# Performance work log

Hardware: AMD Instinct MI355X
Metric: run time of the kernel (lower is better)

Reference implementation:

```python
import jax, jax.numpy as jnp
import numpy as np

GAMMA = 2
EPS = 1e-8  # torch F.cosine_similarity norm clamp


def setup_inputs() -> dict:
    key = jax.random.key(0)
    k1, k2, k3 = jax.random.split(key, 3)
    b, c, h, w = 32, 256, 32, 32
    x = jax.random.normal(k1, (b, c, h, w), dtype=jnp.float32)
    # 1x1 conv transform_net (num_layers=1): weight (c_out, c_in), bias (c_out,)
    conv_w = jax.random.normal(k2, (c, c), dtype=jnp.float32) / np.sqrt(c)
    conv_b = jax.random.normal(k3, (c,), dtype=jnp.float32) * 0.01
    return {"x": x, "conv_w": conv_w, "conv_b": conv_b}


def reference(x, conv_w, conv_b):
    b, c, h, w = x.shape
    hw = h * w
    xf = x.reshape(b, c, hw)  # (b, c, hw)
    # cosine similarity: normalize channels once, then a single GEMM
    norm = jnp.sqrt(jnp.sum(xf * xf, axis=1, keepdims=True))
    xn = xf / jnp.maximum(norm, EPS)
    sim = jnp.einsum('bcq,bck->bqk', xn, xn)  # (b, hw, hw)
    sim = jax.nn.relu(sim) ** GAMMA
    # 1x1 conv transform
    t = jnp.einsum('oc,bck->bok', conv_w, xf) + conv_b[None, :, None]  # (b, c, hw)
    # weighted aggregation: out[b, c, q] = sum_k sim[b, q, k] * t[b, c, k]
    out = jnp.einsum('bqk,bck->bcq', sim, t)
    return out.reshape(b, c, h, w)
```

## Files before the change

### kernel.cpp

```cpp
#include <hip/hip_runtime.h>
#include <math.h>

#define B 32
#define C 256
#define HW 1024

typedef __attribute__((ext_vector_type(8))) short bf16x8;
typedef __attribute__((ext_vector_type(4))) float f32x4;

__device__ __forceinline__ unsigned short f2bf(float f) {
    unsigned int u = __float_as_uint(f);
    u += 0x7fffu + ((u >> 16) & 1u);
    return (unsigned short)(u >> 16);
}

__device__ __forceinline__ void gload16(const void* g, void* l) {
    __builtin_amdgcn_global_load_lds(
        (const __attribute__((address_space(1))) unsigned int*)g,
        (__attribute__((address_space(3))) unsigned int*)l, 16, 0, 0);
}

__global__ __launch_bounds__(256) void prepn_kernel(const float* __restrict__ x,
                                                    float* __restrict__ norm,
                                                    unsigned short* __restrict__ xnT) {
    __shared__ float xt[256][65];
    __shared__ float psum[4][64];
    __shared__ float rn[64];
    const int t = threadIdx.x;
    const int q0 = blockIdx.x * 64, b = blockIdx.y;
    const float* xb = x + (size_t)b * C * HW + q0;
#pragma unroll
    for (int p = 0; p < 16; ++p) {
        int u = p * 256 + t;
        int c = u >> 4, q4 = (u & 15) * 4;
        float4 v = *(const float4*)(xb + (size_t)c * HW + q4);
        xt[c][q4] = v.x; xt[c][q4 + 1] = v.y; xt[c][q4 + 2] = v.z; xt[c][q4 + 3] = v.w;
    }
    __syncthreads();
    {
        int cb = t >> 6, q = t & 63;
        float s = 0.f;
#pragma unroll
        for (int cc = 0; cc < 64; ++cc) {
            float v = xt[cb * 64 + cc][q];
            s += v * v;
        }
        psum[cb][q] = s;
    }
    __syncthreads();
    if (t < 64) {
        float s = psum[0][t] + psum[1][t] + psum[2][t] + psum[3][t];
        float n = fmaxf(sqrtf(s), 1e-8f);
        norm[b * HW + q0 + t] = n;
        rn[t] = 1.f / n;
    }
    __syncthreads();
    unsigned short* xrow = xnT + ((size_t)b * HW + q0) * C;
#pragma unroll
    for (int p = 0; p < 16; ++p) {
        int q = p * 4 + (t >> 6);
        float rnq = rn[q];
#pragma unroll
        for (int i = 0; i < 4; ++i) {
            int c = (t & 63) + 64 * i;
            xrow[(size_t)q * C + c] = f2bf(xt[c][q] * rnq);
        }
    }
}

__global__ __launch_bounds__(256) void castw_kernel(const float* __restrict__ w,
                                                    unsigned short* __restrict__ wb) {
    int i = (blockIdx.x * 256 + threadIdx.x) * 4;
    float4 v = *(const float4*)(w + i);
    unsigned long long pk = (unsigned long long)f2bf(v.x) |
                            ((unsigned long long)f2bf(v.y) << 16) |
                            ((unsigned long long)f2bf(v.z) << 32) |
                            ((unsigned long long)f2bf(v.w) << 48);
    *(unsigned long long*)(wb + i) = pk;
}

__global__ __launch_bounds__(256) void tgemm_kernel(
    const unsigned short* __restrict__ A, const unsigned short* __restrict__ Bm,
    unsigned short* __restrict__ Cb, const float* __restrict__ bias,
    const float* __restrict__ norm) {
    __shared__ unsigned short Asub[128 * 64];
    __shared__ unsigned short Bsub[128 * 64];
    const int t = threadIdx.x;
    const int bz = blockIdx.z;
    const int m0 = blockIdx.y * 128, n0 = blockIdx.x * 128;

    const int ug = ((t & 7) ^ ((t >> 3) & 7)) * 16;
    const char* gA = (const char*)A + (size_t)(m0 + (t >> 3)) * (C * 2) + ug;
    const char* gB = (const char*)(Bm + (size_t)bz * HW * C) +
                     (size_t)(n0 + (t >> 3)) * (C * 2) + ug;
    char* lA = (char*)Asub + t * 16;
    char* lB = (char*)Bsub + t * 16;
    const int rowStep = 32 * C * 2;

    const int lane = t & 63;
    const int wid = t >> 6;
    const int wr = wid >> 1, wc = wid & 1;
    const int lr = lane & 15, hi = lane >> 4;
    int rowA[4], rowB[4], sb[2];
#pragma unroll
    for (int i = 0; i < 4; ++i) rowA[i] = (wr * 64 + i * 16 + lr) * 128;
#pragma unroll
    for (int j = 0; j < 4; ++j) rowB[j] = (wc * 64 + j * 16 + lr) * 128;
#pragma unroll
    for (int kk = 0; kk < 2; ++kk) sb[kk] = ((hi + 4 * kk) ^ (lr & 7)) * 16;

    f32x4 acc[4][4];
#pragma unroll
    for (int i = 0; i < 4; ++i)
#pragma unroll
        for (int j = 0; j < 4; ++j) acc[i][j] = (f32x4)(0.f);

#pragma unroll
    for (int p = 0; p < 4; ++p) {
        gload16(gA + p * rowStep, lA + p * 4096);
        gload16(gB + p * rowStep, lB + p * 4096);
    }
    for (int ks = 0; ks < 4; ++ks) {
        __syncthreads();
#pragma unroll
        for (int kk = 0; kk < 2; ++kk) {
            bf16x8 av[4], bv[4];
#pragma unroll
            for (int i = 0; i < 4; ++i)
                av[i] = *(const bf16x8*)((const char*)Asub + rowA[i] + sb[kk]);
#pragma unroll
            for (int j = 0; j < 4; ++j)
                bv[j] = *(const bf16x8*)((const char*)Bsub + rowB[j] + sb[kk]);
#pragma unroll
            for (int i = 0; i < 4; ++i)
#pragma unroll
                for (int j = 0; j < 4; ++j)
                    acc[i][j] = __builtin_amdgcn_mfma_f32_16x16x32_bf16(
                        av[i], bv[j], acc[i][j], 0, 0, 0);
        }
        __syncthreads();
        if (ks + 1 < 4) {
            const char* gA2 = gA + (size_t)(ks + 1) * 128;
            const char* gB2 = gB + (size_t)(ks + 1) * 128;
#pragma unroll
            for (int p = 0; p < 4; ++p) {
                gload16(gA2 + p * rowStep, lA + p * 4096);
                gload16(gB2 + p * rowStep, lB + p * 4096);
            }
        }
    }
    const int mb = m0 + wr * 64 + hi * 4;
    const int nb = n0 + wc * 64 + lr;
    unsigned short* Cp = Cb + (size_t)bz * C * HW;
    float nrm[4];
#pragma unroll
    for (int j = 0; j < 4; ++j) nrm[j] = norm[bz * HW + nb + j * 16];
#pragma unroll
    for (int i = 0; i < 4; ++i)
#pragma unroll
        for (int r = 0; r < 4; ++r) {
            int m = mb + i * 16 + r;
            float bbv = bias[m];
#pragma unroll
            for (int j = 0; j < 4; ++j)
                Cp[(size_t)m * HW + nb + j * 16] = f2bf(acc[i][j][r] * nrm[j] + bbv);
        }
}

__global__ __launch_bounds__(512, 4) void fused_kernel(
    const unsigned short* __restrict__ xnT,
    const unsigned short* __restrict__ tb,
    float* __restrict__ out) {
    __shared__ unsigned short XQ[64 * 256];
    __shared__ unsigned short XK[128 * 64];
    __shared__ unsigned short SS[64 * 128];
    __shared__ unsigned short TT[256 * 32];
    const int t = threadIdx.x;
    const int wgid = blockIdx.x;
    const int xcd = wgid & 7, g = wgid >> 3;
    const int qt = g & 15, bh = g >> 4;
    const int b = bh * 8 + xcd;
    const int qg0 = qt * 64;

    const int lane = t & 63;
    const int wid = t >> 6;
    const int lr = lane & 15, hi = lane >> 4;
    const int qh = wid & 1, kq = wid >> 1;
    const int cq = wid >> 1;

    const char* xq_g = (const char*)(xnT + ((size_t)b * HW + qg0) * C);
    const char* xk_gb = (const char*)(xnT + (size_t)b * HW * C);
    const char* t_gb = (const char*)(tb + (size_t)b * C * HW);

#pragma unroll
    for (int p = 0; p < 4; ++p) {
        int u = p * 512 + t;
        int q = u >> 5, s = u & 31;
        int sp = (s & 16) | ((s & 15) ^ (q & 15));
        gload16(xq_g + (size_t)q * 512 + sp * 16, (char*)XQ + (size_t)u * 16);
    }

    f32x4 oacc[4][2];
#pragma unroll
    for (int i = 0; i < 4; ++i)
#pragma unroll
        for (int j = 0; j < 2; ++j) oacc[i][j] = (f32x4)(0.f);

    for (int kt = 0; kt < 8; ++kt) {
        const int kg0 = kt * 128;
        f32x4 sacc[2][2];
#pragma unroll
        for (int i = 0; i < 2; ++i)
#pragma unroll
            for (int j = 0; j < 2; ++j) sacc[i][j] = (f32x4)(0.f);

        for (int cch = 0; cch < 4; ++cch) {
            __syncthreads();
#pragma unroll
            for (int p = 0; p < 2; ++p) {
                int u = p * 512 + t;
                int k = u >> 3, s = u & 7;
                int sp = s ^ (k & 7);
                gload16(xk_gb + (size_t)(kg0 + k) * 512 + cch * 128 + sp * 16,
                        (char*)XK + (size_t)u * 16);
            }
            if (cch == 3) {
#pragma unroll
                for (int p = 0; p < 2; ++p) {
                    int u = p * 512 + t;
                    int c = u >> 2, s = u & 3;
                    gload16(t_gb + (size_t)c * 2048 + kg0 * 2 + s * 16,
                            (char*)TT + (size_t)u * 16);
                }
            }
            __syncthreads();
#pragma unroll
            for (int cs = 0; cs < 2; ++cs) {
                bf16x8 av[2], bv[2];
#pragma unroll
                for (int i = 0; i < 2; ++i) {
                    int krow = kq * 32 + i * 16 + lr;
                    int off = (cs * 64 + hi * 16) ^ ((krow & 7) << 4);
                    av[i] = *(const bf16x8*)((const char*)XK + krow * 128 + off);
                }
#pragma unroll
                for (int j = 0; j < 2; ++j) {
                    int qrow = qh * 32 + j * 16 + lr;
                    int off = (cch * 128 + cs * 64 + hi * 16) ^ ((qrow & 15) << 4);
                    bv[j] = *(const bf16x8*)((const char*)XQ + qrow * 512 + off);
                }
#pragma unroll
                for (int i = 0; i < 2; ++i)
#pragma unroll
                    for (int j = 0; j < 2; ++j)
                        sacc[i][j] = __builtin_amdgcn_mfma_f32_16x16x32_bf16(
                            av[i], bv[j], sacc[i][j], 0, 0, 0);
            }
        }

#pragma unroll
        for (int i = 0; i < 2; ++i)
#pragma unroll
            for (int j = 0; j < 2; ++j) {
                int q = qh * 32 + j * 16 + lr;
                int kb = kq * 32 + i * 16 + hi * 4;
                unsigned long long pk = 0;
#pragma unroll
                for (int r = 0; r < 4; ++r) {
                    float v = fmaxf(sacc[i][j][r], 0.f);
                    v = v * v;
                    pk |= (unsigned long long)f2bf(v) << (16 * r);
                }
                int off = (kb * 2) ^ ((q & 15) << 4);
                *(unsigned long long*)((char*)SS + q * 256 + off) = pk;
            }
        __syncthreads();

#pragma unroll
        for (int kc = 0; kc < 4; ++kc) {
            if (kc > 0) {
                __syncthreads();
#pragma unroll
                for (int p = 0; p < 2; ++p) {
                    int u = p * 512 + t;
                    int c = u >> 2, s = u & 3;
                    gload16(t_gb + (size_t)c * 2048 + (kg0 + kc * 32) * 2 + s * 16,
                            (char*)TT + (size_t)u * 16);
                }
                __syncthreads();
            }
            bf16x8 av[4], bv[2];
#pragma unroll
            for (int i = 0; i < 4; ++i) {
                int crow = cq * 64 + i * 16 + lr;
                av[i] = *(const bf16x8*)((const char*)TT + crow * 64 + hi * 16);
            }
#pragma unroll
            for (int j = 0; j < 2; ++j) {
                int qrow = qh * 32 + j * 16 + lr;
                int off = (kc * 64 + hi * 16) ^ ((qrow & 15) << 4);
                bv[j] = *(const bf16x8*)((const char*)SS + qrow * 256 + off);
            }
#pragma unroll
            for (int i = 0; i < 4; ++i)
#pragma unroll
                for (int j = 0; j < 2; ++j)
                    oacc[i][j] = __builtin_amdgcn_mfma_f32_16x16x32_bf16(
                        av[i], bv[j], oacc[i][j], 0, 0, 0);
        }
    }

#pragma unroll
    for (int i = 0; i < 4; ++i)
#pragma unroll
        for (int r = 0; r < 4; ++r) {
            int c = cq * 64 + i * 16 + hi * 4 + r;
            float* op = out + ((size_t)b * C + c) * HW + qg0 + qh * 32 + lr;
#pragma unroll
            for (int j = 0; j < 2; ++j) op[j * 16] = oacc[i][j][r];
        }
}

extern "C" void kernel_launch(void* const* d_in, const int* in_sizes, int n_in,
                              void* d_out, int out_size, void* d_ws, size_t ws_size,
                              hipStream_t stream) {
    const float* x    = (const float*)d_in[0];
    const float* w    = (const float*)d_in[1];
    const float* bias = (const float*)d_in[2];
    float* out = (float*)d_out;

    char* ws = (char*)d_ws;
    float* norm         = (float*)ws;
    unsigned short* wbf = (unsigned short*)(ws + (128 << 10));
    unsigned short* xnT = (unsigned short*)(ws + (256 << 10));
    unsigned short* tb  = (unsigned short*)(ws + (256 << 10) + (16u << 20));

    hipLaunchKernelGGL(prepn_kernel, dim3(HW / 64, B), dim3(256), 0, stream,
                       x, norm, xnT);
    hipLaunchKernelGGL(castw_kernel, dim3(C * C / 1024), dim3(256), 0, stream, w, wbf);
    hipLaunchKernelGGL(tgemm_kernel, dim3(HW / 128, C / 128, B), dim3(256), 0, stream,
                       wbf, xnT, tb, bias, norm);
    hipLaunchKernelGGL(fused_kernel, dim3((HW / 64) * B), dim3(512), 0, stream,
                       xnT, tb, out);
}
```

Measured before the change: 76.74 us.

## Double-buffer XK staging and load T fragments directly into registers

Splits the XK shared tile into two buffers so the next channel chunk (and the next key tile's first chunk) is prefetched while MFMAs run on the current one. This removes one barrier per chunk. The TT shared-memory staging of the transformed features is dropped; each wave instead loads its T fragments for all four k-chunks straight from global memory into registers. The output tile is remapped so each wave owns 32 channels across all 64 queries. This cuts barriers in the aggregation phase but adds strided global loads and more register pressure.

Measured after the change: 78.94 us. +2.9%, slower.

```diff
diff --git a/kernel.cpp b/kernel.cpp
--- a/kernel.cpp
+++ b/kernel.cpp
@@ -172,9 +172,9 @@
     const unsigned short* __restrict__ tb,
     float* __restrict__ out) {
     __shared__ unsigned short XQ[64 * 256];
-    __shared__ unsigned short XK[128 * 64];
+    __shared__ unsigned short XK0[128 * 64];
+    __shared__ unsigned short XK1[128 * 64];
     __shared__ unsigned short SS[64 * 128];
-    __shared__ unsigned short TT[256 * 32];
     const int t = threadIdx.x;
     const int wgid = blockIdx.x;
     const int xcd = wgid & 7, g = wgid >> 3;
@@ -186,11 +186,21 @@
     const int wid = t >> 6;
     const int lr = lane & 15, hi = lane >> 4;
     const int qh = wid & 1, kq = wid >> 1;
-    const int cq = wid >> 1;
 
     const char* xq_g = (const char*)(xnT + ((size_t)b * HW + qg0) * C);
     const char* xk_gb = (const char*)(xnT + (size_t)b * HW * C);
     const char* t_gb = (const char*)(tb + (size_t)b * C * HW);
+
+    auto stage_xk = [&](int kg0, int cch, char* dst) {
+#pragma unroll
+        for (int p = 0; p < 2; ++p) {
+            int u = p * 512 + t;
+            int k = u >> 3, s = u & 7;
+            int sp = s ^ (k & 7);
+            gload16(xk_gb + (size_t)(kg0 + k) * 512 + cch * 128 + sp * 16,
+                    dst + u * 16);
+        }
+    };
 
 #pragma unroll
     for (int p = 0; p < 4; ++p) {
@@ -199,12 +209,13 @@
         int sp = (s & 16) | ((s & 15) ^ (q & 15));
         gload16(xq_g + (size_t)q * 512 + sp * 16, (char*)XQ + (size_t)u * 16);
     }
-
-    f32x4 oacc[4][2];
-#pragma unroll
-    for (int i = 0; i < 4; ++i)
-#pragma unroll
-        for (int j = 0; j < 2; ++j) oacc[i][j] = (f32x4)(0.f);
+    stage_xk(0, 0, (char*)XK0);
+
+    f32x4 oacc[2][4];
+#pragma unroll
+    for (int i = 0; i < 2; ++i)
+#pragma unroll
+        for (int j = 0; j < 4; ++j) oacc[i][j] = (f32x4)(0.f);
 
     for (int kt = 0; kt < 8; ++kt) {
         const int kg0 = kt * 128;
@@ -214,26 +225,13 @@
 #pragma unroll
             for (int j = 0; j < 2; ++j) sacc[i][j] = (f32x4)(0.f);
 
+#pragma unroll
         for (int cch = 0; cch < 4; ++cch) {
             __syncthreads();
-#pragma unroll
-            for (int p = 0; p < 2; ++p) {
-                int u = p * 512 + t;
-                int k = u >> 3, s = u & 7;
-                int sp = s ^ (k & 7);
-                gload16(xk_gb + (size_t)(kg0 + k) * 512 + cch * 128 + sp * 16,
-                        (char*)XK + (size_t)u * 16);
-            }
-            if (cch == 3) {
-#pragma unroll
-                for (int p = 0; p < 2; ++p) {
-                    int u = p * 512 + t;
-                    int c = u >> 2, s = u & 3;
-                    gload16(t_gb + (size_t)c * 2048 + kg0 * 2 + s * 16,
-                            (char*)TT + (size_t)u * 16);
-                }
-            }
-            __syncthreads();
+            char* nbuf = (cch & 1) ? (char*)XK0 : (char*)XK1;
+            if (cch < 3) stage_xk(kg0, cch + 1, nbuf);
+            else         stage_xk(kt < 7 ? kg0 + 128 : kg0, 0, (char*)XK0);
+            const char* xk = (cch & 1) ? (const char*)XK1 : (const char*)XK0;
 #pragma unroll
             for (int cs = 0; cs < 2; ++cs) {
                 bf16x8 av[2], bv[2];
@@ -241,7 +239,7 @@
                 for (int i = 0; i < 2; ++i) {
                     int krow = kq * 32 + i * 16 + lr;
                     int off = (cs * 64 + hi * 16) ^ ((krow & 7) << 4);
-                    av[i] = *(const bf16x8*)((const char*)XK + krow * 128 + off);
+                    av[i] = *(const bf16x8*)(xk + krow * 128 + off);
                 }
 #pragma unroll
                 for (int j = 0; j < 2; ++j) {
@@ -276,48 +274,40 @@
             }
         __syncthreads();
 
+        bf16x8 tt[2][4];
+#pragma unroll
+        for (int i = 0; i < 2; ++i)
+#pragma unroll
+            for (int kc = 0; kc < 4; ++kc)
+                tt[i][kc] = *(const bf16x8*)(
+                    t_gb + (size_t)(wid * 32 + i * 16 + lr) * 2048 +
+                    (kg0 + kc * 32 + hi * 8) * 2);
 #pragma unroll
         for (int kc = 0; kc < 4; ++kc) {
-            if (kc > 0) {
-                __syncthreads();
-#pragma unroll
-                for (int p = 0; p < 2; ++p) {
-                    int u = p * 512 + t;
-                    int c = u >> 2, s = u & 3;
-                    gload16(t_gb + (size_t)c * 2048 + (kg0 + kc * 32) * 2 + s * 16,
-                            (char*)TT + (size_t)u * 16);
-                }
-                __syncthreads();
-            }
-            bf16x8 av[4], bv[2];
-#pragma unroll
-            for (int i = 0; i < 4; ++i) {
-                int crow = cq * 64 + i * 16 + lr;
-                av[i] = *(const bf16x8*)((const char*)TT + crow * 64 + hi * 16);
-            }
-#pragma unroll
-            for (int j = 0; j < 2; ++j) {
-                int qrow = qh * 32 + j * 16 + lr;
+            bf16x8 bv[4];
+#pragma unroll
+            for (int j = 0; j < 4; ++j) {
+                int qrow = j * 16 + lr;
                 int off = (kc * 64 + hi * 16) ^ ((qrow & 15) << 4);
                 bv[j] = *(const bf16x8*)((const char*)SS + qrow * 256 + off);
             }
 #pragma unroll
-            for (int i = 0; i < 4; ++i)
-#pragma unroll
-                for (int j = 0; j < 2; ++j)
+            for (int i = 0; i < 2; ++i)
+#pragma unroll
+                for (int j = 0; j < 4; ++j)
                     oacc[i][j] = __builtin_amdgcn_mfma_f32_16x16x32_bf16(
-                        av[i], bv[j], oacc[i][j], 0, 0, 0);
-        }
-    }
-
-#pragma unroll
-    for (int i = 0; i < 4; ++i)
+                        tt[i][kc], bv[j], oacc[i][j], 0, 0, 0);
+        }
+    }
+
+#pragma unroll
+    for (int i = 0; i < 2; ++i)
 #pragma unroll
         for (int r = 0; r < 4; ++r) {
-            int c = cq * 64 + i * 16 + hi * 4 + r;
-            float* op = out + ((size_t)b * C + c) * HW + qg0 + qh * 32 + lr;
-#pragma unroll
-            for (int j = 0; j < 2; ++j) op[j * 16] = oacc[i][j][r];
+            int c = wid * 32 + i * 16 + hi * 4 + r;
+            float* op = out + ((size_t)b * C + c) * HW + qg0 + lr;
+#pragma unroll
+            for (int j = 0; j < 4; ++j) op[j * 16] = oacc[i][j][r];
         }
 }
 
```
